# Kernel optimization log

Hardware: AMD Instinct MI355X
Metric: run time of the kernel (lower is better)

## Reference

```python
import jax, jax.numpy as jnp
import numpy as np

H = 256          # hidden_dim
K = 5            # num_mixtures
Z = 32           # latent_dim
A = 3            # action dim
B, T = 128, 512
IN = Z + A       # LSTM input features
MDN = K * (1 + 2 * Z)  # 325


def setup_inputs() -> dict:
    key = jax.random.key(0)
    ks = jax.random.split(key, 8)
    s_in = 1.0 / np.sqrt(IN)
    s_h = 1.0 / np.sqrt(H)
    return {
        "z_t": jax.random.normal(ks[0], (B, T, Z), jnp.float32),
        "a_t": jax.random.normal(ks[1], (B, T, A), jnp.float32),
        # LSTM params: fused gate kernels, gate order [i, f, g, o]
        "Wx": jax.random.normal(ks[2], (IN, 4 * H), jnp.float32) * s_in,
        "Wh": jax.random.normal(ks[3], (H, 4 * H), jnp.float32) * s_h,
        "b": jnp.zeros((4 * H,), jnp.float32),
        # MDN head Dense(325)
        "Wd": jax.random.normal(ks[4], (H, MDN), jnp.float32) * s_h,
        "bd": jnp.zeros((MDN,), jnp.float32),
    }


def _mdnrnn(z_t, a_t, Wx, Wh, b, Wd, bd):
    x = jnp.concatenate([z_t, a_t], axis=-1)          # (B,T,IN)
    # hoist the input projection out of the recurrence (same math)
    xproj = jnp.einsum("bti,ig->btg", x, Wx)          # (B,T,4H)
    xproj_t = jnp.swapaxes(xproj, 0, 1)               # (T,B,4H)
    bsz = x.shape[0]
    c0 = jnp.zeros((bsz, H), x.dtype)
    h0 = jnp.zeros((bsz, H), x.dtype)

    def step(carry, xp):
        c, h = carry
        gates = xp + h @ Wh + b                        # (B,4H)
        i, f, g, o = jnp.split(gates, 4, axis=-1)
        i = jax.nn.sigmoid(i)
        f = jax.nn.sigmoid(f)
        g = jnp.tanh(g)
        o = jax.nn.sigmoid(o)
        c = f * c + i * g
        h = o * jnp.tanh(c)
        return (c, h), h

    final_carry, hs = jax.lax.scan(step, (c0, h0), xproj_t)
    outputs = jnp.swapaxes(hs, 0, 1)                  # (B,T,H)

    mdn = outputs @ Wd + bd                           # (B,T,325)
    log_pi, mu, log_sigma = jnp.split(mdn, [K, K + K * Z * 2 // 2 + K * Z - K], axis=-1)
    # splits: [K, (1+Z)*K] -> log_pi (K), mu (K*Z), log_sigma (K*Z)
    log_pi, mu, log_sigma = mdn[..., :K], mdn[..., K:K + K * Z], mdn[..., K + K * Z:]
    bt = outputs.shape[:2]
    mu = mu.reshape(bt[0], bt[1], K, Z)
    log_sigma = log_sigma.reshape(bt[0], bt[1], K, Z)
    log_pi = jax.nn.log_softmax(log_pi, axis=-1)
    sigma = jnp.exp(log_sigma) + 1e-06
    return log_pi, mu, sigma, final_carry


def reference(z_t, a_t, Wx, Wh, b, Wd, bd):
    return _mdnrnn(z_t, a_t, Wx, Wh, b, Wd, bd)
```

## Files before the change

### kernel.cpp

```cpp
#include <hip/hip_runtime.h>
#include <hip/hip_bf16.h>
#include <math.h>

#define T_LEN 512
#define B_SZ  128
#define H_DIM 256
#define G_DIM 1024
#define IN_D  35
#define MDN_D 325
#define K_MIX 5

#define NSLICE 4
#define BG     2
#define NGRP   64

static constexpr long OFF_MU    = 327680L;
static constexpr long OFF_SIGMA = 10813440L;
static constexpr long OFF_C     = 21299200L;
static constexpr long OFF_H     = 21331968L;

static constexpr size_t WS_OUT = 0;
static constexpr size_t WS_HG  = 33554432;

__device__ __forceinline__ float fast_sigmoid(float x) { return 1.0f / (1.0f + __expf(-x)); }
__device__ __forceinline__ float fast_tanh(float x) {
    return 1.0f - 2.0f / (__expf(2.0f * x) + 1.0f);
}

__global__ __launch_bounds__(512) void lstm4_kernel(
    const float* __restrict__ z_t, const float* __restrict__ a_t,
    const float* __restrict__ Wx,  const float* __restrict__ Wh,
    const float* __restrict__ bias,
    float* __restrict__ h_glb,
    __hip_bfloat16* __restrict__ outs,
    float* __restrict__ out_c, float* __restrict__ out_h)
{
    const int bid = blockIdx.x;
    const int gr  = bid & 63;
    const int s   = bid >> 6;
    const int tid = threadIdx.x;
    const int cg  = tid >> 2;
    const int kq  = tid & 3;
    const int lc0 = cg * 2;
    const int gate = lc0 >> 6;
    const int j0   = lc0 & 63;
    const int gcol0 = gate * 256 + s * 64 + j0;

    __shared__ __align__(16) float h_lds[BG][4][68];
    __shared__ __align__(16) float x_lds[BG][36];
    __shared__ __align__(16) float g_red[BG][256];

    for (int i = tid; i < BG * 4 * 68; i += 512) ((float*)h_lds)[i] = 0.0f;
    if (tid < BG) x_lds[tid][35] = 0.0f;

    float W0[64], W1[64];
    #pragma unroll
    for (int i = 0; i < 64; ++i) {
        const size_t r = (size_t)(kq * 64 + i) * G_DIM;
        W0[i] = Wh[r + gcol0];
        W1[i] = Wh[r + gcol0 + 1];
    }
    float X0[9], X1[9];
    #pragma unroll
    for (int i = 0; i < 9; ++i) {
        int xk = kq * 9 + i;
        bool ok = (xk < IN_D);
        X0[i] = ok ? Wx[(size_t)xk * G_DIM + gcol0]     : 0.0f;
        X1[i] = ok ? Wx[(size_t)xk * G_DIM + gcol0 + 1] : 0.0f;
    }

    const int cb = tid >> 6;
    const int cj = tid & 63;
    const float bc0 = bias[0 * 256 + s * 64 + cj];
    const float bc1 = bias[1 * 256 + s * 64 + cj];
    const float bc2 = bias[2 * 256 + s * 64 + cj];
    const float bc3 = bias[3 * 256 + s * 64 + cj];
    float c_reg = 0.0f;

    const int batch0 = gr * BG;
    float* hg = h_glb + (size_t)gr * (2 * BG * H_DIM);

    __syncthreads();

    for (int t = 0; t < T_LEN; ++t) {
        if (tid >= 128 && tid < 192) {
            int q = tid - 128, b = q >> 5, k = q & 31;
            x_lds[b][k] = z_t[((size_t)(batch0 + b) * T_LEN + t) * 32 + k];
        } else if (tid >= 192 && tid < 192 + BG * 3) {
            int q = tid - 192, b = (q >= 3), k = q - 3 * b;
            x_lds[b][32 + k] = a_t[((size_t)(batch0 + b) * T_LEN + t) * 3 + k];
        }

        if (t > 0) {
            const unsigned want = (unsigned)((t - 1) & 3);
            const float* ap = hg + ((t - 1) & 1) * (BG * H_DIM) + tid;
            unsigned u;
            do {
                asm volatile("global_load_dword %0, %1, off sc0 sc1\n\t"
                             "s_waitcnt vmcnt(0)"
                             : "=v"(u) : "v"(ap) : "memory");
            } while ((u & 3u) != want);
            int b = tid >> 8, k = tid & 255;
            h_lds[b][k >> 6][k & 63] = __uint_as_float(u);
        }
        __syncthreads();

        float a00 = 0.0f, a01 = 0.0f, a10 = 0.0f, a11 = 0.0f;
        {
            const float4* hp0 = (const float4*)h_lds[0][kq];
            const float4* hp1 = (const float4*)h_lds[1][kq];
            #pragma unroll
            for (int i4 = 0; i4 < 16; ++i4) {
                float4 hv0 = hp0[i4];
                float4 hv1 = hp1[i4];
                a00 = fmaf(hv0.x, W0[4*i4+0], a00); a01 = fmaf(hv0.x, W1[4*i4+0], a01);
                a10 = fmaf(hv1.x, W0[4*i4+0], a10); a11 = fmaf(hv1.x, W1[4*i4+0], a11);
                a00 = fmaf(hv0.y, W0[4*i4+1], a00); a01 = fmaf(hv0.y, W1[4*i4+1], a01);
                a10 = fmaf(hv1.y, W0[4*i4+1], a10); a11 = fmaf(hv1.y, W1[4*i4+1], a11);
                a00 = fmaf(hv0.z, W0[4*i4+2], a00); a01 = fmaf(hv0.z, W1[4*i4+2], a01);
                a10 = fmaf(hv1.z, W0[4*i4+2], a10); a11 = fmaf(hv1.z, W1[4*i4+2], a11);
                a00 = fmaf(hv0.w, W0[4*i4+3], a00); a01 = fmaf(hv0.w, W1[4*i4+3], a01);
                a10 = fmaf(hv1.w, W0[4*i4+3], a10); a11 = fmaf(hv1.w, W1[4*i4+3], a11);
            }
            const float* xp0 = &x_lds[0][kq * 9];
            const float* xp1 = &x_lds[1][kq * 9];
            #pragma unroll
            for (int i = 0; i < 9; ++i) {
                float xv0 = xp0[i], xv1 = xp1[i];
                a00 = fmaf(xv0, X0[i], a00); a01 = fmaf(xv0, X1[i], a01);
                a10 = fmaf(xv1, X0[i], a10); a11 = fmaf(xv1, X1[i], a11);
            }
        }
        a00 += __shfl_xor(a00, 1, 64); a00 += __shfl_xor(a00, 2, 64);
        a01 += __shfl_xor(a01, 1, 64); a01 += __shfl_xor(a01, 2, 64);
        a10 += __shfl_xor(a10, 1, 64); a10 += __shfl_xor(a10, 2, 64);
        a11 += __shfl_xor(a11, 1, 64); a11 += __shfl_xor(a11, 2, 64);
        if (kq == 0) {
            g_red[0][lc0] = a00; g_red[0][lc0 + 1] = a01;
            g_red[1][lc0] = a10; g_red[1][lc0 + 1] = a11;
        }
        __syncthreads();

        if (tid < 128) {
            float gi = g_red[cb][      cj] + bc0;
            float gf = g_red[cb][ 64 + cj] + bc1;
            float gg = g_red[cb][128 + cj] + bc2;
            float go = g_red[cb][192 + cj] + bc3;
            float iv = fast_sigmoid(gi), fv = fast_sigmoid(gf), ov = fast_sigmoid(go);
            float gv = fast_tanh(gg);
            c_reg = fmaf(fv, c_reg, iv * gv);
            float hv = ov * fast_tanh(c_reg);
            unsigned u = (__float_as_uint(hv) & ~3u) | (unsigned)(t & 3);
            float* dst = hg + (t & 1) * (BG * H_DIM) + cb * H_DIM + s * 64 + cj;
            asm volatile("global_store_dword %0, %1, off sc0 sc1"
                         :: "v"(dst), "v"(u) : "memory");
            outs[((size_t)(batch0 + cb) * T_LEN + t) * H_DIM + s * 64 + cj] =
                __float2bfloat16(hv);
            if (t == T_LEN - 1) {
                out_c[(batch0 + cb) * H_DIM + s * 64 + cj] = c_reg;
                out_h[(batch0 + cb) * H_DIM + s * 64 + cj] = hv;
            }
        }
    }
}

__global__ __launch_bounds__(256, 1) void mdn_kernel(
    const unsigned short* __restrict__ outputs, const float* __restrict__ Wd,
    const float* __restrict__ bd, float* __restrict__ out)
{
    __shared__ __align__(16) float hT[H_DIM * 16];
    __shared__ float lp[16][K_MIX];

    const int tid = threadIdx.x;
    const long row0 = (long)blockIdx.x * 16;

    for (int idx = tid; idx < H_DIM * 16; idx += 256) {
        int r = idx >> 8;
        int k = idx & (H_DIM - 1);
        unsigned int u = outputs[(row0 + r) * H_DIM + k];
        hT[k * 16 + r] = __uint_as_float(u << 16);
    }
    __syncthreads();

    const int  cA = tid;
    const int  cB = tid + 256;
    const bool vB = (cB < MDN_D);
    const float bA = bd[cA];
    const float bB = vB ? bd[cB] : 0.0f;
    float accA[16], accB[16];
    #pragma unroll
    for (int r = 0; r < 16; ++r) { accA[r] = bA; accB[r] = bB; }

    for (int k = 0; k < H_DIM; ++k) {
        float wA = Wd[(size_t)k * MDN_D + cA];
        float wB = vB ? Wd[(size_t)k * MDN_D + cB] : 0.0f;
        const float4* hp = (const float4*)(hT + k * 16);
        float4 h0 = hp[0], h1 = hp[1], h2 = hp[2], h3 = hp[3];
        float hr[16] = { h0.x,h0.y,h0.z,h0.w, h1.x,h1.y,h1.z,h1.w,
                         h2.x,h2.y,h2.z,h2.w, h3.x,h3.y,h3.z,h3.w };
        #pragma unroll
        for (int r = 0; r < 16; ++r) {
            accA[r] = fmaf(hr[r], wA, accA[r]);
            accB[r] = fmaf(hr[r], wB, accB[r]);
        }
    }

    float* out_mu = out + OFF_MU;
    float* out_sg = out + OFF_SIGMA;
    #pragma unroll
    for (int r = 0; r < 16; ++r) {
        long row = row0 + r;
        float v = accA[r];
        if (cA < K_MIX)            lp[r][cA] = v;
        else if (cA < K_MIX + 160) out_mu[row * 160 + (cA - K_MIX)] = v;
        else                       out_sg[row * 160 + (cA - 165)]   = __expf(v) + 1e-6f;
        if (vB)                    out_sg[row * 160 + (cB - 165)]   = __expf(accB[r]) + 1e-6f;
    }
    __syncthreads();

    if (tid < 16) {
        int r = tid;
        long row = row0 + r;
        float v0 = lp[r][0], v1 = lp[r][1], v2 = lp[r][2], v3 = lp[r][3], v4 = lp[r][4];
        float m = fmaxf(fmaxf(fmaxf(v0, v1), fmaxf(v2, v3)), v4);
        float sum = __expf(v0-m) + __expf(v1-m) + __expf(v2-m) + __expf(v3-m) + __expf(v4-m);
        float ls = m + __logf(sum);
        out[row*5 + 0] = v0 - ls;
        out[row*5 + 1] = v1 - ls;
        out[row*5 + 2] = v2 - ls;
        out[row*5 + 3] = v3 - ls;
        out[row*5 + 4] = v4 - ls;
    }
}

extern "C" void kernel_launch(void* const* d_in, const int* in_sizes, int n_in,
                              void* d_out, int out_size, void* d_ws, size_t ws_size,
                              hipStream_t stream)
{
    const float* z_t = (const float*)d_in[0];
    const float* a_t = (const float*)d_in[1];
    const float* Wx  = (const float*)d_in[2];
    const float* Wh  = (const float*)d_in[3];
    const float* b   = (const float*)d_in[4];
    const float* Wd  = (const float*)d_in[5];
    const float* bd  = (const float*)d_in[6];
    float* out = (float*)d_out;

    char* ws = (char*)d_ws;
    __hip_bfloat16* outs = (__hip_bfloat16*)(ws + WS_OUT);
    float* h_glb         = (float*)(ws + WS_HG);

    lstm4_kernel<<<NGRP * NSLICE, 512, 0, stream>>>(z_t, a_t, Wx, Wh, b,
                                                    h_glb, outs,
                                                    out + OFF_C, out + OFF_H);
    mdn_kernel<<<(B_SZ * T_LEN) / 16, 256, 0, stream>>>((const unsigned short*)outs,
                                                        Wd, bd, out);
}
```

Before: 1.259 ms.

## Poll only remote h slices with dwordx2 and prefetch next-step inputs

Each block now writes its own freshly computed h slice straight into LDS. The global spin-poll covers only the 192 remote slices, using 192 threads with 64-bit loads instead of 512 single-dword loads. Loading the next timestep's z/a input is moved to the end of the step, using threads that do not poll, so it overlaps with the barrier wait. This aims to cut the latency of the cross-block recurrence handshake. In exchange, the LDS writes and the x_lds prefetch now rely on ordering with the existing barriers.

```diff
diff --git a/kernel.cpp b/kernel.cpp
--- a/kernel.cpp
+++ b/kernel.cpp
@@ -22,12 +22,14 @@
 static constexpr size_t WS_OUT = 0;
 static constexpr size_t WS_HG  = 33554432;
 
+typedef unsigned uint2v __attribute__((ext_vector_type(2)));
+
 __device__ __forceinline__ float fast_sigmoid(float x) { return 1.0f / (1.0f + __expf(-x)); }
 __device__ __forceinline__ float fast_tanh(float x) {
     return 1.0f - 2.0f / (__expf(2.0f * x) + 1.0f);
 }
 
-__global__ __launch_bounds__(512) void lstm4_kernel(
+__global__ __launch_bounds__(512, 1) void lstm5_kernel(
     const float* __restrict__ z_t, const float* __restrict__ a_t,
     const float* __restrict__ Wx,  const float* __restrict__ Wh,
     const float* __restrict__ bias,
@@ -77,31 +79,37 @@
     const float bc3 = bias[3 * 256 + s * 64 + cj];
     float c_reg = 0.0f;
 
+    const int q  = tid - 128;
+    const int pb = (q >= 96) ? 1 : 0;
+    const int pp = q - 96 * pb;
+    const int pk0 = pp * 2;
+    const int pkk = pk0 + ((pk0 >= s * 64) ? 64 : 0);
+
     const int batch0 = gr * BG;
     float* hg = h_glb + (size_t)gr * (2 * BG * H_DIM);
 
+    if (tid >= 384 && tid < 448) {
+        int qq = tid - 384, b = qq >> 5, k = qq & 31;
+        x_lds[b][k] = z_t[((size_t)(batch0 + b) * T_LEN + 0) * 32 + k];
+    } else if (tid >= 448 && tid < 448 + BG * 3) {
+        int qq = tid - 448, b = (qq >= 3), k = qq - 3 * b;
+        x_lds[b][32 + k] = a_t[((size_t)(batch0 + b) * T_LEN + 0) * 3 + k];
+    }
     __syncthreads();
 
     for (int t = 0; t < T_LEN; ++t) {
-        if (tid >= 128 && tid < 192) {
-            int q = tid - 128, b = q >> 5, k = q & 31;
-            x_lds[b][k] = z_t[((size_t)(batch0 + b) * T_LEN + t) * 32 + k];
-        } else if (tid >= 192 && tid < 192 + BG * 3) {
-            int q = tid - 192, b = (q >= 3), k = q - 3 * b;
-            x_lds[b][32 + k] = a_t[((size_t)(batch0 + b) * T_LEN + t) * 3 + k];
-        }
-
-        if (t > 0) {
+        if (t > 0 && tid >= 128 && tid < 320) {
             const unsigned want = (unsigned)((t - 1) & 3);
-            const float* ap = hg + ((t - 1) & 1) * (BG * H_DIM) + tid;
-            unsigned u;
+            const float* ap = hg + ((t - 1) & 1) * (BG * H_DIM) + pb * H_DIM + pkk;
+            uint2v u;
             do {
-                asm volatile("global_load_dword %0, %1, off sc0 sc1\n\t"
+                asm volatile("global_load_dwordx2 %0, %1, off sc0 sc1\n\t"
                              "s_waitcnt vmcnt(0)"
                              : "=v"(u) : "v"(ap) : "memory");
-            } while ((u & 3u) != want);
-            int b = tid >> 8, k = tid & 255;
-            h_lds[b][k >> 6][k & 63] = __uint_as_float(u);
+            } while ((u.x & 3u) != want || (u.y & 3u) != want);
+            float* dst = &h_lds[pb][pkk >> 6][pkk & 63];
+            dst[0] = __uint_as_float(u.x);
+            dst[1] = __uint_as_float(u.y);
         }
         __syncthreads();
 
@@ -154,11 +162,21 @@
             float* dst = hg + (t & 1) * (BG * H_DIM) + cb * H_DIM + s * 64 + cj;
             asm volatile("global_store_dword %0, %1, off sc0 sc1"
                          :: "v"(dst), "v"(u) : "memory");
+            h_lds[cb][s][cj] = __uint_as_float(u);
             outs[((size_t)(batch0 + cb) * T_LEN + t) * H_DIM + s * 64 + cj] =
                 __float2bfloat16(hv);
             if (t == T_LEN - 1) {
                 out_c[(batch0 + cb) * H_DIM + s * 64 + cj] = c_reg;
                 out_h[(batch0 + cb) * H_DIM + s * 64 + cj] = hv;
+            }
+        }
+        if (t + 1 < T_LEN) {
+            if (tid >= 384 && tid < 448) {
+                int qq = tid - 384, b = qq >> 5, k = qq & 31;
+                x_lds[b][k] = z_t[((size_t)(batch0 + b) * T_LEN + (t + 1)) * 32 + k];
+            } else if (tid >= 448 && tid < 448 + BG * 3) {
+                int qq = tid - 448, b = (qq >= 3), k = qq - 3 * b;
+                x_lds[b][32 + k] = a_t[((size_t)(batch0 + b) * T_LEN + (t + 1)) * 3 + k];
             }
         }
     }
@@ -250,7 +268,7 @@
     __hip_bfloat16* outs = (__hip_bfloat16*)(ws + WS_OUT);
     float* h_glb         = (float*)(ws + WS_HG);
 
-    lstm4_kernel<<<NGRP * NSLICE, 512, 0, stream>>>(z_t, a_t, Wx, Wh, b,
+    lstm5_kernel<<<NGRP * NSLICE, 512, 0, stream>>>(z_t, a_t, Wx, Wh, b,
                                                     h_glb, outs,
                                                     out + OFF_C, out + OFF_H);
     mdn_kernel<<<(B_SZ * T_LEN) / 16, 256, 0, stream>>>((const unsigned short*)outs,
```

Measured after the change: 1.206 ms. -4.2%, faster.
